# Optimization experiments

Measured on AMD Instinct MI355X. Metric: run time of the kernel, lower is better.

The kernel has to match this reference:

```python
import jax, jax.numpy as jnp
import numpy as np

TOPK_OUTER = 15  # hard-coded k in topk_loss
TOPK_INNER = 4   # self.topk


def avgpool2x2(x, t):
    # t applications of 2x2/stride-2 average pooling on NCHW
    for _ in range(t):
        B, C, H, W = x.shape
        x = x.reshape(B, C, H // 2, 2, W // 2, 2).mean(axis=(3, 5))
    return x


def flatten_chw(x):
    # NCHW -> [B*H*W, C]
    B, C, H, W = x.shape
    return jnp.transpose(x, (0, 2, 3, 1)).reshape(-1, C)


def cosine_similar(q, p):
    # inner product divided by outer product of L2 norms (as in source)
    inner = jnp.einsum('ik,sk->is', q, p)
    qn = jnp.sqrt(jnp.einsum('ik,ik->i', q, q))
    pn = jnp.sqrt(jnp.einsum('sk,sk->s', p, p))
    return inner / (qn[:, None] * pn[None, :])


def setup_inputs() -> dict:
    key = jax.random.key(0)
    kq, ks = jax.random.split(key)
    q = jax.random.normal(kq, (64, 512, 32, 32), dtype=jnp.float32)
    S = jax.random.normal(ks, (128, 512, 32, 32), dtype=jnp.float32)
    return {"q": q, "S": S}


def reference(q, S):
    C = S.shape[1]
    qf = flatten_chw(avgpool2x2(q, 2))                 # [Nq, C]
    s_src = flatten_chw(avgpool2x2(S, 2))              # [Ns2, C]
    s1 = flatten_chw(avgpool2x2(S, 1))                 # [Ns1, C]
    s_all = jnp.concatenate([s1, s_src], axis=0)       # [Ns, C]
    sim = cosine_similar(qf, s_all)                    # [Nq, Ns]
    q2s, _ = jax.lax.top_k(sim, TOPK_OUTER)            # [Nq, 15]
    probs = jax.nn.softmax(q2s, axis=-1)
    topk_v, _ = jax.lax.top_k(probs, TOPK_INNER)       # [Nq, 4]
    loss = -jnp.log(topk_v).mean(axis=-1).mean()
    return loss
```

## Files before the change

kernel.cpp:

```cpp
#include <hip/hip_runtime.h>
#include <hip/hip_bf16.h>
#include <stdint.h>

#define NQ 4096
#define NS 40960
#define CDIM 512
#define QT 256
#define SC 64
#define NSPLIT 32
#define SPER (NS / NSPLIT)
#define NCHUNK (SPER / SC)
#define NCAND 960

typedef float f32x16 __attribute__((ext_vector_type(16)));
typedef unsigned int u32x4 __attribute__((ext_vector_type(4)));
typedef unsigned int u32x2 __attribute__((ext_vector_type(2)));

__device__ __forceinline__ unsigned short f2bf(float f) {
    uint32_t u = __builtin_bit_cast(uint32_t, f);
    u += 0x7fffu + ((u >> 16) & 1u);
    return (unsigned short)(u >> 16);
}
__device__ __forceinline__ float bf2f(unsigned short u) {
    uint32_t x = ((uint32_t)u) << 16;
    return __builtin_bit_cast(float, x);
}
__device__ __forceinline__ int kperm(int c) {
    return (c & ~24) | ((c & 8) << 1) | ((c & 16) >> 1);
}

__device__ __forceinline__ void async_load16(const void* g, void* l) {
    auto gp = reinterpret_cast<const __attribute__((address_space(1))) uint32_t*>(
        reinterpret_cast<uintptr_t>(g));
    auto lp = reinterpret_cast<__attribute__((address_space(3))) uint32_t*>(
        reinterpret_cast<uintptr_t>(l));
    __builtin_amdgcn_global_load_lds(gp, lp, 16 , 0, 0);
}

__device__ __forceinline__ void ins15(float (&r)[15], float v) {
#pragma unroll
    for (int i = 14; i >= 1; --i) r[i] = __builtin_amdgcn_fmed3f(v, r[i - 1], r[i]);
    r[0] = fmaxf(r[0], v);
}

__global__ __launch_bounds__(256) void pool_q_norm(const float* __restrict__ q,
                                                   char* __restrict__ qn) {
    int bb = blockIdx.x >> 3, h = blockIdx.x & 7;
    int t = threadIdx.x, lane = t & 63, wid = t >> 6;
    float vals[2][8];
    float ss[8] = {0, 0, 0, 0, 0, 0, 0, 0};
#pragma unroll
    for (int e = 0; e < 2; ++e) {
        int c = 2 * t + e;
        const float* base = q + ((size_t)(bb * 512 + c) * 1024 + 4 * h * 32);
#pragma unroll
        for (int w2 = 0; w2 < 8; ++w2) vals[e][w2] = 0.f;
#pragma unroll
        for (int i = 0; i < 4; ++i) {
            const float4* row = (const float4*)(base + i * 32);
#pragma unroll
            for (int w2 = 0; w2 < 8; ++w2) {
                float4 v = row[w2];
                vals[e][w2] += (v.x + v.y) + (v.z + v.w);
            }
        }
#pragma unroll
        for (int w2 = 0; w2 < 8; ++w2) {
            vals[e][w2] *= (1.f / 16.f);
            ss[w2] += vals[e][w2] * vals[e][w2];
        }
    }
    __shared__ float red[8][4];
#pragma unroll
    for (int k = 0; k < 8; ++k) {
        float v = ss[k];
#pragma unroll
        for (int o = 32; o > 0; o >>= 1) v += __shfl_xor(v, o, 64);
        if (lane == 0) red[k][wid] = v;
    }
    __syncthreads();
    int cp = kperm(2 * t);
#pragma unroll
    for (int w2 = 0; w2 < 8; ++w2) {
        float inv = rsqrtf(red[w2][0] + red[w2][1] + red[w2][2] + red[w2][3]);
        int p = __builtin_amdgcn_cvt_pk_fp8_f32(vals[0][w2] * inv, vals[1][w2] * inv, 0, false);
        *(unsigned short*)(qn + (size_t)(bb * 64 + h * 8 + w2) * 512 + cp) = (unsigned short)(p & 0xffff);
    }
}

__global__ __launch_bounds__(256) void pool_s_norm(const float* __restrict__ S,
                                                   char* __restrict__ sn) {
    int bb = blockIdx.x >> 3, h2 = blockIdx.x & 7;
    int t = threadIdx.x, lane = t & 63, wid = t >> 6;
    __shared__ unsigned short tile[40 * 512];
    __shared__ float rowsum[40];
#pragma unroll
    for (int e = 0; e < 2; ++e) {
        int c = 2 * t + e;
        const float* base = S + ((size_t)(bb * 512 + c) * 1024 + 4 * h2 * 32);
        float s1v[2][16];
#pragma unroll
        for (int j = 0; j < 2; ++j) {
            const float4* r0 = (const float4*)(base + (2 * j) * 32);
            const float4* r1 = (const float4*)(base + (2 * j + 1) * 32);
#pragma unroll
            for (int f = 0; f < 8; ++f) {
                float4 a = r0[f], b2 = r1[f];
                s1v[j][2 * f]     = (a.x + a.y + b2.x + b2.y) * 0.25f;
                s1v[j][2 * f + 1] = (a.z + a.w + b2.z + b2.w) * 0.25f;
            }
        }
#pragma unroll
        for (int j = 0; j < 2; ++j)
#pragma unroll
            for (int w1 = 0; w1 < 16; ++w1)
                tile[(j * 16 + w1) * 512 + c] = f2bf(s1v[j][w1]);
#pragma unroll
        for (int w2 = 0; w2 < 8; ++w2) {
            float src = (s1v[0][2 * w2] + s1v[0][2 * w2 + 1] +
                         s1v[1][2 * w2] + s1v[1][2 * w2 + 1]) * 0.25f;
            tile[(32 + w2) * 512 + c] = f2bf(src);
        }
    }
    __syncthreads();
#pragma unroll
    for (int k = 0; k < 10; ++k) {
        int row = 4 * k + wid;
        u32x4 d = *(const u32x4*)(&tile[row * 512 + lane * 8]);
        float s = 0.f;
#pragma unroll
        for (int j = 0; j < 4; ++j) {
            float x0 = bf2f((unsigned short)(d[j] & 0xffffu));
            float x1 = bf2f((unsigned short)(d[j] >> 16));
            s += x0 * x0 + x1 * x1;
        }
#pragma unroll
        for (int o = 32; o > 0; o >>= 1) s += __shfl_xor(s, o, 64);
        if (lane == 0) rowsum[row] = s;
    }
    __syncthreads();
#pragma unroll
    for (int k = 0; k < 10; ++k) {
        int idx = t + 256 * k;
        int r = idx >> 6, seg = idx & 63;
        float inv = rsqrtf(rowsum[r]);
        const unsigned short* src = &tile[r * 512 + seg * 8];
        float x[8];
#pragma unroll
        for (int m = 0; m < 8; ++m) x[m] = bf2f(src[m]) * inv;
        unsigned int w0 = (unsigned int)__builtin_amdgcn_cvt_pk_fp8_f32(
            x[2], x[3], __builtin_amdgcn_cvt_pk_fp8_f32(x[0], x[1], 0, false), true);
        unsigned int w1 = (unsigned int)__builtin_amdgcn_cvt_pk_fp8_f32(
            x[6], x[7], __builtin_amdgcn_cvt_pk_fp8_f32(x[4], x[5], 0, false), true);
        int nseg = (seg & ~3) | ((seg & 1) << 1) | ((seg >> 1) & 1);
        int grow = (r < 32) ? (bb * 256 + (2 * h2 + (r >> 4)) * 16 + (r & 15))
                            : (32768 + bb * 64 + h2 * 8 + (r - 32));
        uint2 o2; o2.x = w0; o2.y = w1;
        *(uint2*)(sn + (size_t)grow * 512 + nseg * 8) = o2;
    }
}

__global__ __launch_bounds__(256, 2) void sim_topk(const char* __restrict__ qn,
                                                   const char* __restrict__ sn,
                                                   float* __restrict__ partial) {
    __shared__ char Bs[2][SC * 512];
    int id = blockIdx.x;
    int xcd = id & 7, j = id >> 3;
    int y = xcd * 4 + (j & 3);
    int x = j >> 2;
    int tid = threadIdx.x, lane = tid & 63, wid = tid >> 6;
    int rlo = lane & 31, hi = lane >> 5;
    int qbase = x * QT + wid * 64;
    int sbase = y * SPER;
    char* BsB = &Bs[0][0];

    u32x4 b[2][16];
#pragma unroll
    for (int g = 0; g < 2; ++g) {
        const char* qp = qn + (size_t)(qbase + g * 32 + rlo) * 512 + hi * 16;
#pragma unroll
        for (int kk = 0; kk < 16; ++kk) b[g][kk] = *(const u32x4*)(qp + kk * 32);
    }

    float r0[15], r1[15];
#pragma unroll
    for (int i = 0; i < 15; ++i) { r0[i] = -2.0f; r1[i] = -2.0f; }

    auto stage = [&](int ch, int buf) {
#pragma unroll
        for (int ii = 0; ii < 8; ++ii) {
            int i = wid * 8 + ii;
            int row = 2 * i + hi;
            size_t srcoff = (size_t)(sbase + ch * SC + row) * 512
                          + (size_t)((rlo ^ (row & 31)) * 16);
            async_load16(sn + srcoff, BsB + buf * 32768 + i * 1024);
        }
    };

    stage(0, 0);
    stage(1, 1);
    for (int ch = 0; ch < NCHUNK; ++ch) {
        int buf = ch & 1;
        asm volatile("s_waitcnt vmcnt(8)" ::: "memory");
        __builtin_amdgcn_s_barrier();
#pragma unroll
        for (int g = 0; g < 2; ++g)
#pragma unroll
            for (int kk = 0; kk < 16; ++kk) asm volatile("" : "+v"(b[g][kk]));
        const char* B0 = BsB + buf * 32768;
        f32x16 a00, a01, a10, a11;
#pragma unroll
        for (int e = 0; e < 16; ++e) { a00[e] = 0.f; a01[e] = 0.f; a10[e] = 0.f; a11[e] = 0.f; }
        __builtin_amdgcn_s_setprio(1);
#pragma unroll
        for (int kk = 0; kk < 16; ++kk) {
            int slot = ((kk * 2 + hi) ^ rlo) * 16;
            u32x4 aA = *(const u32x4*)(B0 + rlo * 512 + slot);
            u32x4 aB = *(const u32x4*)(B0 + (32 + rlo) * 512 + slot);
            long aAlo = __builtin_bit_cast(long, (u32x2){aA[0], aA[1]});
            long aAhi = __builtin_bit_cast(long, (u32x2){aA[2], aA[3]});
            long aBlo = __builtin_bit_cast(long, (u32x2){aB[0], aB[1]});
            long aBhi = __builtin_bit_cast(long, (u32x2){aB[2], aB[3]});
            long b0lo = __builtin_bit_cast(long, (u32x2){b[0][kk][0], b[0][kk][1]});
            long b0hi = __builtin_bit_cast(long, (u32x2){b[0][kk][2], b[0][kk][3]});
            long b1lo = __builtin_bit_cast(long, (u32x2){b[1][kk][0], b[1][kk][1]});
            long b1hi = __builtin_bit_cast(long, (u32x2){b[1][kk][2], b[1][kk][3]});
            a00 = __builtin_amdgcn_mfma_f32_32x32x16_fp8_fp8(aAlo, b0lo, a00, 0, 0, 0);
            a01 = __builtin_amdgcn_mfma_f32_32x32x16_fp8_fp8(aAlo, b1lo, a01, 0, 0, 0);
            a10 = __builtin_amdgcn_mfma_f32_32x32x16_fp8_fp8(aBlo, b0lo, a10, 0, 0, 0);
            a11 = __builtin_amdgcn_mfma_f32_32x32x16_fp8_fp8(aBlo, b1lo, a11, 0, 0, 0);
            a00 = __builtin_amdgcn_mfma_f32_32x32x16_fp8_fp8(aAhi, b0hi, a00, 0, 0, 0);
            a01 = __builtin_amdgcn_mfma_f32_32x32x16_fp8_fp8(aAhi, b1hi, a01, 0, 0, 0);
            a10 = __builtin_amdgcn_mfma_f32_32x32x16_fp8_fp8(aBhi, b0hi, a10, 0, 0, 0);
            a11 = __builtin_amdgcn_mfma_f32_32x32x16_fp8_fp8(aBhi, b1hi, a11, 0, 0, 0);
        }
        __builtin_amdgcn_s_setprio(0);
        __builtin_amdgcn_s_barrier();
        { int n = ch + 2; if (n >= NCHUNK) n -= NCHUNK; stage(n, buf); }
#pragma unroll
        for (int e = 0; e < 16; ++e) {
            float v;
            v = a00[e]; if (__any(v > r0[14])) ins15(r0, v);
            v = a10[e]; if (__any(v > r0[14])) ins15(r0, v);
            v = a01[e]; if (__any(v > r1[14])) ins15(r1, v);
            v = a11[e]; if (__any(v > r1[14])) ins15(r1, v);
        }
    }

    int q0 = qbase + rlo;
    float* dst0 = partial + (((size_t)q0 * NSPLIT + y) * 2 + hi) * 15;
    float* dst1 = partial + (((size_t)(q0 + 32) * NSPLIT + y) * 2 + hi) * 15;
#pragma unroll
    for (int i = 0; i < 15; ++i) { dst0[i] = r0[i]; dst1[i] = r1[i]; }
}

__global__ __launch_bounds__(256) void topk_loss(const float* __restrict__ partial,
                                                 float* __restrict__ accum) {
    int t = threadIdx.x, lane = t & 63, wid = t >> 6;
    int r = blockIdx.x * 4 + wid;
    const float* src = partial + (size_t)r * NCAND;
    float v[15];
#pragma unroll
    for (int i = 0; i < 15; ++i) v[i] = src[lane + 64 * i];
    float m0 = 0.f, sexp = 0.f, top4 = 0.f;
#pragma unroll
    for (int round = 0; round < 15; ++round) {
        float m = v[0];
        int mi = lane * 16;
#pragma unroll
        for (int i = 1; i < 15; ++i)
            if (v[i] > m) { m = v[i]; mi = lane * 16 + i; }
#pragma unroll
        for (int o = 32; o > 0; o >>= 1) {
            float om = __shfl_xor(m, o, 64);
            int oi = __shfl_xor(mi, o, 64);
            if (om > m || (om == m && oi < mi)) { m = om; mi = oi; }
        }
        int wl = mi >> 4, wi = mi & 15;
#pragma unroll
        for (int i = 0; i < 15; ++i)
            if (i == wi && wl == lane) v[i] = -1e30f;
        if (round == 0) m0 = m;
        sexp += expf(m - m0);
        if (round < 4) top4 += m;
    }
    float loss = m0 + logf(sexp) - 0.25f * top4;
    __shared__ float red[4];
    if (lane == 0) red[wid] = loss;
    __syncthreads();
    if (t == 0) atomicAdd(accum, red[0] + red[1] + red[2] + red[3]);
}

__global__ void finalize_out(const float* __restrict__ accum, float* __restrict__ out) {
    out[0] = accum[0] * (1.0f / (float)NQ);
}

extern "C" void kernel_launch(void* const* d_in, const int* in_sizes, int n_in,
                              void* d_out, int out_size, void* d_ws, size_t ws_size,
                              hipStream_t stream) {
    (void)in_sizes; (void)n_in; (void)out_size; (void)ws_size;
    const float* q = (const float*)d_in[0];
    const float* S = (const float*)d_in[1];
    char* ws = (char*)d_ws;
    char* qn = ws;
    char* sn = ws + 2097152;
    float* partial = (float*)(ws + 2097152 + 20971520);
    float* accum   = (float*)(ws + 2097152 + 20971520 + 15728640);

    hipMemsetAsync(accum, 0, 4, stream);
    pool_q_norm<<<512, 256, 0, stream>>>(q, qn);
    pool_s_norm<<<1024, 256, 0, stream>>>(S, sn);
    sim_topk<<<512, 256, 0, stream>>>(qn, sn, partial);
    topk_loss<<<NQ / 4, 256, 0, stream>>>(partial, accum);
    finalize_out<<<1, 1, 0, stream>>>(accum, (float*)d_out);
}
```

Measured before the change: 324.3 us.

## Quantize to FP4 with scaled MFMA and overlap top-k insertion with compute

The normalized query and support features are now quantized to packed FP4 (e2m1) with a power-of-two prescale instead of FP8. The similarity GEMM uses the scaled f8f6f4 32x32x64 MFMA, which halves operand bytes and LDS traffic. The main loop switches to triple buffering with 32-row chunks, and top-15 insertion of the previous chunk's results is interleaved with the current chunk's MFMAs. The old per-value wave-vote early-out is gone, so every value now goes through the insertion network, which adds VALU work. FP4's coarse levels also risk changing which candidates land in the top-15.

```diff
diff --git a/kernel.cpp b/kernel.cpp
--- a/kernel.cpp
+++ b/kernel.cpp
@@ -6,7 +6,7 @@
 #define NS 40960
 #define CDIM 512
 #define QT 256
-#define SC 64
+#define SC 32
 #define NSPLIT 32
 #define SPER (NS / NSPLIT)
 #define NCHUNK (SPER / SC)
@@ -14,7 +14,8 @@
 
 typedef float f32x16 __attribute__((ext_vector_type(16)));
 typedef unsigned int u32x4 __attribute__((ext_vector_type(4)));
-typedef unsigned int u32x2 __attribute__((ext_vector_type(2)));
+typedef int i32x4 __attribute__((ext_vector_type(4)));
+typedef int i32x8 __attribute__((ext_vector_type(8)));
 
 __device__ __forceinline__ unsigned short f2bf(float f) {
     uint32_t u = __builtin_bit_cast(uint32_t, f);
@@ -25,8 +26,13 @@
     uint32_t x = ((uint32_t)u) << 16;
     return __builtin_bit_cast(float, x);
 }
-__device__ __forceinline__ int kperm(int c) {
-    return (c & ~24) | ((c & 8) << 1) | ((c & 16) >> 1);
+
+__device__ __forceinline__ unsigned fp4enc(float y) {
+    float m = fabsf(y);
+    unsigned c = (m < 0.25f) ? 0u : (m < 0.75f) ? 1u : (m < 1.25f) ? 2u
+               : (m < 1.75f) ? 3u : (m < 2.5f)  ? 4u : (m < 3.5f)  ? 5u
+               : (m < 5.0f)  ? 6u : 7u;
+    return c | ((__builtin_bit_cast(unsigned, y) >> 28) & 8u);
 }
 
 __device__ __forceinline__ void async_load16(const void* g, void* l) {
@@ -44,7 +50,7 @@
 }
 
 __global__ __launch_bounds__(256) void pool_q_norm(const float* __restrict__ q,
-                                                   char* __restrict__ qn) {
+                                                   unsigned char* __restrict__ qn) {
     int bb = blockIdx.x >> 3, h = blockIdx.x & 7;
     int t = threadIdx.x, lane = t & 63, wid = t >> 6;
     float vals[2][8];
@@ -79,17 +85,17 @@
         if (lane == 0) red[k][wid] = v;
     }
     __syncthreads();
-    int cp = kperm(2 * t);
 #pragma unroll
     for (int w2 = 0; w2 < 8; ++w2) {
-        float inv = rsqrtf(red[w2][0] + red[w2][1] + red[w2][2] + red[w2][3]);
-        int p = __builtin_amdgcn_cvt_pk_fp8_f32(vals[0][w2] * inv, vals[1][w2] * inv, 0, false);
-        *(unsigned short*)(qn + (size_t)(bb * 64 + h * 8 + w2) * 512 + cp) = (unsigned short)(p & 0xffff);
+        float inv16 = rsqrtf(red[w2][0] + red[w2][1] + red[w2][2] + red[w2][3]) * 16.f;
+        unsigned e0 = fp4enc(vals[0][w2] * inv16);
+        unsigned e1 = fp4enc(vals[1][w2] * inv16);
+        qn[(size_t)(bb * 64 + h * 8 + w2) * 256 + t] = (unsigned char)(e0 | (e1 << 4));
     }
 }
 
 __global__ __launch_bounds__(256) void pool_s_norm(const float* __restrict__ S,
-                                                   char* __restrict__ sn) {
+                                                   unsigned char* __restrict__ sn) {
     int bb = blockIdx.x >> 3, h2 = blockIdx.x & 7;
     int t = threadIdx.x, lane = t & 63, wid = t >> 6;
     __shared__ unsigned short tile[40 * 512];
@@ -143,27 +149,22 @@
     for (int k = 0; k < 10; ++k) {
         int idx = t + 256 * k;
         int r = idx >> 6, seg = idx & 63;
-        float inv = rsqrtf(rowsum[r]);
+        float inv16 = rsqrtf(rowsum[r]) * 16.f;
         const unsigned short* src = &tile[r * 512 + seg * 8];
-        float x[8];
-#pragma unroll
-        for (int m = 0; m < 8; ++m) x[m] = bf2f(src[m]) * inv;
-        unsigned int w0 = (unsigned int)__builtin_amdgcn_cvt_pk_fp8_f32(
-            x[2], x[3], __builtin_amdgcn_cvt_pk_fp8_f32(x[0], x[1], 0, false), true);
-        unsigned int w1 = (unsigned int)__builtin_amdgcn_cvt_pk_fp8_f32(
-            x[6], x[7], __builtin_amdgcn_cvt_pk_fp8_f32(x[4], x[5], 0, false), true);
-        int nseg = (seg & ~3) | ((seg & 1) << 1) | ((seg >> 1) & 1);
+        unsigned out = 0;
+#pragma unroll
+        for (int m = 0; m < 8; ++m)
+            out |= fp4enc(bf2f(src[m]) * inv16) << (4 * m);
         int grow = (r < 32) ? (bb * 256 + (2 * h2 + (r >> 4)) * 16 + (r & 15))
                             : (32768 + bb * 64 + h2 * 8 + (r - 32));
-        uint2 o2; o2.x = w0; o2.y = w1;
-        *(uint2*)(sn + (size_t)grow * 512 + nseg * 8) = o2;
-    }
-}
-
-__global__ __launch_bounds__(256, 2) void sim_topk(const char* __restrict__ qn,
-                                                   const char* __restrict__ sn,
+        *(unsigned*)(sn + (size_t)grow * 256 + seg * 4) = out;
+    }
+}
+
+__global__ __launch_bounds__(256, 2) void sim_topk(const unsigned char* __restrict__ qn,
+                                                   const unsigned char* __restrict__ sn,
                                                    float* __restrict__ partial) {
-    __shared__ char Bs[2][SC * 512];
+    __shared__ char Bs[3][SC * 256];
     int id = blockIdx.x;
     int xcd = id & 7, j = id >> 3;
     int y = xcd * 4 + (j & 3);
@@ -174,12 +175,12 @@
     int sbase = y * SPER;
     char* BsB = &Bs[0][0];
 
-    u32x4 b[2][16];
+    u32x4 b[2][8];
 #pragma unroll
     for (int g = 0; g < 2; ++g) {
-        const char* qp = qn + (size_t)(qbase + g * 32 + rlo) * 512 + hi * 16;
-#pragma unroll
-        for (int kk = 0; kk < 16; ++kk) b[g][kk] = *(const u32x4*)(qp + kk * 32);
+        const unsigned char* qp = qn + (size_t)(qbase + g * 32 + rlo) * 256 + hi * 16;
+#pragma unroll
+        for (int kk = 0; kk < 8; ++kk) b[g][kk] = *(const u32x4*)(qp + kk * 32);
     }
 
     float r0[15], r1[15];
@@ -188,64 +189,80 @@
 
     auto stage = [&](int ch, int buf) {
 #pragma unroll
-        for (int ii = 0; ii < 8; ++ii) {
-            int i = wid * 8 + ii;
-            int row = 2 * i + hi;
-            size_t srcoff = (size_t)(sbase + ch * SC + row) * 512
-                          + (size_t)((rlo ^ (row & 31)) * 16);
-            async_load16(sn + srcoff, BsB + buf * 32768 + i * 1024);
-        }
+        for (int ii = 0; ii < 2; ++ii) {
+            int g = (wid * 2 + ii) * 64 + lane;
+            int row = g >> 4, s = g & 15;
+            size_t srcoff = (size_t)(sbase + ch * SC + row) * 256
+                          + (size_t)((s ^ (row & 15)) << 4);
+            async_load16(sn + srcoff, BsB + buf * 8192 + (g << 4));
+        }
+    };
+
+    auto kstep = [&](const char* B0, int kk, f32x16& acc0, f32x16& acc1) {
+        int s0 = kk * 2 + hi;
+        u32x4 a4 = *(const u32x4*)(B0 + rlo * 256 + ((s0 ^ (rlo & 15)) << 4));
+        i32x4 ai = __builtin_bit_cast(i32x4, a4);
+        i32x8 a = __builtin_shufflevector(ai, (i32x4){0, 0, 0, 0}, 0, 1, 2, 3, 4, 5, 6, 7);
+        i32x8 b0 = __builtin_shufflevector(__builtin_bit_cast(i32x4, b[0][kk]),
+                                           (i32x4){0, 0, 0, 0}, 0, 1, 2, 3, 4, 5, 6, 7);
+        i32x8 b1 = __builtin_shufflevector(__builtin_bit_cast(i32x4, b[1][kk]),
+                                           (i32x4){0, 0, 0, 0}, 0, 1, 2, 3, 4, 5, 6, 7);
+        acc0 = __builtin_amdgcn_mfma_scale_f32_32x32x64_f8f6f4(
+            a, b0, acc0, 4, 4, 0, 0x7B7B7B7B, 0, 0x7B7B7B7B);
+        acc1 = __builtin_amdgcn_mfma_scale_f32_32x32x64_f8f6f4(
+            a, b1, acc1, 4, 4, 0, 0x7B7B7B7B, 0, 0x7B7B7B7B);
     };
 
     stage(0, 0);
     stage(1, 1);
-    for (int ch = 0; ch < NCHUNK; ++ch) {
-        int buf = ch & 1;
-        asm volatile("s_waitcnt vmcnt(8)" ::: "memory");
+    f32x16 cA0, cA1, pB0, pB1;
+#pragma unroll
+    for (int e = 0; e < 16; ++e) { pB0[e] = -2.0f; pB1[e] = -2.0f; }
+    int bufR = 0, bufS = 2, chS = 2;
+
+    for (int it = 0; it < NCHUNK / 2; ++it) {
+        asm volatile("s_waitcnt vmcnt(2)" ::: "memory");
         __builtin_amdgcn_s_barrier();
+        stage(chS, bufS);
+        chS = (chS + 1 == NCHUNK) ? 0 : chS + 1;
+        bufS = (bufS + 1 == 3) ? 0 : bufS + 1;
 #pragma unroll
         for (int g = 0; g < 2; ++g)
 #pragma unroll
-            for (int kk = 0; kk < 16; ++kk) asm volatile("" : "+v"(b[g][kk]));
-        const char* B0 = BsB + buf * 32768;
-        f32x16 a00, a01, a10, a11;
-#pragma unroll
-        for (int e = 0; e < 16; ++e) { a00[e] = 0.f; a01[e] = 0.f; a10[e] = 0.f; a11[e] = 0.f; }
-        __builtin_amdgcn_s_setprio(1);
-#pragma unroll
-        for (int kk = 0; kk < 16; ++kk) {
-            int slot = ((kk * 2 + hi) ^ rlo) * 16;
-            u32x4 aA = *(const u32x4*)(B0 + rlo * 512 + slot);
-            u32x4 aB = *(const u32x4*)(B0 + (32 + rlo) * 512 + slot);
-            long aAlo = __builtin_bit_cast(long, (u32x2){aA[0], aA[1]});
-            long aAhi = __builtin_bit_cast(long, (u32x2){aA[2], aA[3]});
-            long aBlo = __builtin_bit_cast(long, (u32x2){aB[0], aB[1]});
-            long aBhi = __builtin_bit_cast(long, (u32x2){aB[2], aB[3]});
-            long b0lo = __builtin_bit_cast(long, (u32x2){b[0][kk][0], b[0][kk][1]});
-            long b0hi = __builtin_bit_cast(long, (u32x2){b[0][kk][2], b[0][kk][3]});
-            long b1lo = __builtin_bit_cast(long, (u32x2){b[1][kk][0], b[1][kk][1]});
-            long b1hi = __builtin_bit_cast(long, (u32x2){b[1][kk][2], b[1][kk][3]});
-            a00 = __builtin_amdgcn_mfma_f32_32x32x16_fp8_fp8(aAlo, b0lo, a00, 0, 0, 0);
-            a01 = __builtin_amdgcn_mfma_f32_32x32x16_fp8_fp8(aAlo, b1lo, a01, 0, 0, 0);
-            a10 = __builtin_amdgcn_mfma_f32_32x32x16_fp8_fp8(aBlo, b0lo, a10, 0, 0, 0);
-            a11 = __builtin_amdgcn_mfma_f32_32x32x16_fp8_fp8(aBlo, b1lo, a11, 0, 0, 0);
-            a00 = __builtin_amdgcn_mfma_f32_32x32x16_fp8_fp8(aAhi, b0hi, a00, 0, 0, 0);
-            a01 = __builtin_amdgcn_mfma_f32_32x32x16_fp8_fp8(aAhi, b1hi, a01, 0, 0, 0);
-            a10 = __builtin_amdgcn_mfma_f32_32x32x16_fp8_fp8(aBhi, b0hi, a10, 0, 0, 0);
-            a11 = __builtin_amdgcn_mfma_f32_32x32x16_fp8_fp8(aBhi, b1hi, a11, 0, 0, 0);
-        }
-        __builtin_amdgcn_s_setprio(0);
+            for (int kk = 0; kk < 8; ++kk) asm volatile("" : "+v"(b[g][kk]));
+        const char* B0 = BsB + bufR * 8192;
+        bufR = (bufR + 1 == 3) ? 0 : bufR + 1;
+#pragma unroll
+        for (int e = 0; e < 16; ++e) { cA0[e] = 0.f; cA1[e] = 0.f; }
+#pragma unroll
+        for (int kk = 0; kk < 8; ++kk) {
+            kstep(B0, kk, cA0, cA1);
+            ins15(r0, pB0[2 * kk]);
+            ins15(r0, pB0[2 * kk + 1]);
+            ins15(r1, pB1[2 * kk]);
+            ins15(r1, pB1[2 * kk + 1]);
+        }
+
+        asm volatile("s_waitcnt vmcnt(2)" ::: "memory");
         __builtin_amdgcn_s_barrier();
-        { int n = ch + 2; if (n >= NCHUNK) n -= NCHUNK; stage(n, buf); }
-#pragma unroll
-        for (int e = 0; e < 16; ++e) {
-            float v;
-            v = a00[e]; if (__any(v > r0[14])) ins15(r0, v);
-            v = a10[e]; if (__any(v > r0[14])) ins15(r0, v);
-            v = a01[e]; if (__any(v > r1[14])) ins15(r1, v);
-            v = a11[e]; if (__any(v > r1[14])) ins15(r1, v);
-        }
-    }
+        stage(chS, bufS);
+        chS = (chS + 1 == NCHUNK) ? 0 : chS + 1;
+        bufS = (bufS + 1 == 3) ? 0 : bufS + 1;
+        const char* B1 = BsB + bufR * 8192;
+        bufR = (bufR + 1 == 3) ? 0 : bufR + 1;
+#pragma unroll
+        for (int e = 0; e < 16; ++e) { pB0[e] = 0.f; pB1[e] = 0.f; }
+#pragma unroll
+        for (int kk = 0; kk < 8; ++kk) {
+            kstep(B1, kk, pB0, pB1);
+            ins15(r0, cA0[2 * kk]);
+            ins15(r0, cA0[2 * kk + 1]);
+            ins15(r1, cA1[2 * kk]);
+            ins15(r1, cA1[2 * kk + 1]);
+        }
+    }
+#pragma unroll
+    for (int e = 0; e < 16; ++e) { ins15(r0, pB0[e]); ins15(r1, pB1[e]); }
 
     int q0 = qbase + rlo;
     float* dst0 = partial + (((size_t)q0 * NSPLIT + y) * 2 + hi) * 15;
@@ -302,10 +319,10 @@
     const float* q = (const float*)d_in[0];
     const float* S = (const float*)d_in[1];
     char* ws = (char*)d_ws;
-    char* qn = ws;
-    char* sn = ws + 2097152;
-    float* partial = (float*)(ws + 2097152 + 20971520);
-    float* accum   = (float*)(ws + 2097152 + 20971520 + 15728640);
+    unsigned char* qn = (unsigned char*)ws;
+    unsigned char* sn = (unsigned char*)(ws + 1048576);
+    float* partial = (float*)(ws + 1048576 + 10485760);
+    float* accum   = (float*)(ws + 1048576 + 10485760 + 15728640);
 
     hipMemsetAsync(accum, 0, 4, stream);
     pool_q_norm<<<512, 256, 0, stream>>>(q, qn);
```

Result: faster. 264.2 us (-18.5%).
